# Optimization experiments

Measured on AMD Instinct MI355X. Metric: run time of the kernel, lower is better.

## Reference

```python
import jax, jax.numpy as jnp
import numpy as np

N_NODES = 50000
N_EDGES = 800000
IN_DIM = 9
HIDDEN = 256
N_CAND = 4096


def setup_inputs() -> dict:
    key = jax.random.key(0)
    ks = jax.random.split(key, 12)
    x = jax.random.normal(ks[0], (N_NODES, IN_DIM), dtype=jnp.float32)
    edge_index = jax.random.randint(ks[1], (2, N_EDGES), 0, N_NODES, dtype=jnp.int64)
    candidate_indices = jax.random.randint(ks[2], (N_CAND,), 0, N_NODES, dtype=jnp.int64)
    # GCNConv weights (glorot-ish scale) and biases
    W1 = jax.random.normal(ks[3], (IN_DIM, HIDDEN), dtype=jnp.float32) / np.sqrt(IN_DIM)
    b1 = jnp.zeros((HIDDEN,), dtype=jnp.float32)
    W2 = jax.random.normal(ks[4], (HIDDEN, HIDDEN), dtype=jnp.float32) / np.sqrt(HIDDEN)
    b2 = jnp.zeros((HIDDEN,), dtype=jnp.float32)
    # score head: Linear(hidden,hidden) -> Tanh -> Linear(hidden,1)
    Wh1 = jax.random.normal(ks[5], (HIDDEN, HIDDEN), dtype=jnp.float32) / np.sqrt(HIDDEN)
    bh1 = jnp.zeros((HIDDEN,), dtype=jnp.float32)
    Wh2 = jax.random.normal(ks[6], (HIDDEN, 1), dtype=jnp.float32) / np.sqrt(HIDDEN)
    bh2 = jnp.zeros((1,), dtype=jnp.float32)
    return {"x": x, "W1": W1, "b1": b1, "W2": W2, "b2": b2,
            "Wh1": Wh1, "bh1": bh1, "Wh2": Wh2, "bh2": bh2,
            "edge_index": edge_index, "candidate_indices": candidate_indices}


def _gcn_norm(edge_index, n_nodes):
    # PyG GCNConv default: add self-loops, symmetric normalization D^-1/2 (A+I) D^-1/2
    loop = jnp.arange(n_nodes, dtype=edge_index.dtype)
    src = jnp.concatenate([edge_index[0], loop])
    dst = jnp.concatenate([edge_index[1], loop])
    deg = jax.ops.segment_sum(jnp.ones_like(dst, dtype=jnp.float32), dst,
                              num_segments=n_nodes)
    dinv = jnp.where(deg > 0, jax.lax.rsqrt(deg), 0.0)
    norm = dinv[src] * dinv[dst]  # [E+N]
    return src, dst, norm


def _gcn_layer(h, src, dst, norm, W, b, n_nodes):
    m = h @ W                              # [N, H] dense GEMM first (fewer edge features)
    msg = m[src] * norm[:, None]           # gather + scale: [E+N, H]
    agg = jax.ops.segment_sum(msg, dst, num_segments=n_nodes)  # scatter-add
    return jax.nn.relu(agg + b)


def reference(x, W1, b1, W2, b2, Wh1, bh1, Wh2, bh2, edge_index, candidate_indices):
    n = x.shape[0]
    src, dst, norm = _gcn_norm(edge_index, n)
    h = _gcn_layer(x, src, dst, norm, W1, b1, n)
    h = _gcn_layer(h, src, dst, norm, W2, b2, n)
    cand_h = h[candidate_indices]                       # [K, H]
    scores = (jnp.tanh(cand_h @ Wh1 + bh1) @ Wh2 + bh2).squeeze(-1)  # [K]
    return scores
```

## Files before the change

### kernel.cpp

```cpp
#include <hip/hip_runtime.h>
#include <math.h>

#define N_NODES 50000
#define N_EDGES 800000
#define IN_DIM  9
#define HIDDEN  256
#define N_CAND  4096

#define SCAN_TPB 256
#define SCAN_NB  ((N_NODES + SCAN_TPB - 1) / SCAN_TPB)


__global__ void hist_kernel(const int* __restrict__ dst, int* __restrict__ cnt) {
    int base = (blockIdx.x * blockDim.x + threadIdx.x) * 4;
    if (base >= N_EDGES) return;
    int4 d4 = *(const int4*)(dst + base);
    atomicAdd(&cnt[d4.x], 1);
    atomicAdd(&cnt[d4.y], 1);
    atomicAdd(&cnt[d4.z], 1);
    atomicAdd(&cnt[d4.w], 1);
}

__global__ __launch_bounds__(SCAN_TPB) void scan1_kernel(const int* __restrict__ cnt,
                                                         int* __restrict__ row_ptr,
                                                         int* __restrict__ blockSums) {
    __shared__ int s[SCAN_TPB];
    int t = threadIdx.x;
    int i = blockIdx.x * SCAN_TPB + t;
    int v = (i < N_NODES) ? cnt[i] : 0;
    s[t] = v;
    __syncthreads();
#pragma unroll
    for (int off = 1; off < SCAN_TPB; off <<= 1) {
        int u = (t >= off) ? s[t - off] : 0;
        __syncthreads();
        s[t] += u;
        __syncthreads();
    }
    if (i < N_NODES) row_ptr[i] = s[t] - v;
    if (t == SCAN_TPB - 1) blockSums[blockIdx.x] = s[t];
}

__global__ __launch_bounds__(SCAN_TPB) void scan2_kernel(const int* __restrict__ blockSums,
                                                         int* __restrict__ blockOff,
                                                         int* __restrict__ row_ptr) {
    __shared__ int s[SCAN_TPB];
    int t = threadIdx.x;
    int v = (t < SCAN_NB) ? blockSums[t] : 0;
    s[t] = v;
    __syncthreads();
#pragma unroll
    for (int off = 1; off < SCAN_TPB; off <<= 1) {
        int u = (t >= off) ? s[t - off] : 0;
        __syncthreads();
        s[t] += u;
        __syncthreads();
    }
    if (t < SCAN_NB) blockOff[t] = s[t] - v;
    if (t == SCAN_TPB - 1) row_ptr[N_NODES] = s[t];
}

__global__ __launch_bounds__(SCAN_TPB) void scan3_kernel(const int* __restrict__ cnt,
                                                         const int* __restrict__ blockOff,
                                                         int* __restrict__ row_ptr,
                                                         int* __restrict__ cur,
                                                         float* __restrict__ dinv) {
    int i = blockIdx.x * SCAN_TPB + threadIdx.x;
    if (i < N_NODES) {
        int rp = row_ptr[i] + blockOff[blockIdx.x];
        row_ptr[i] = rp;
        cur[i] = rp;
        dinv[i] = 1.0f / sqrtf((float)(cnt[i] + 1));
    }
}

__global__ void fill_kernel(const int* __restrict__ srcv, const int* __restrict__ dstv,
                            int* __restrict__ cur, int* __restrict__ col) {
    int base = (blockIdx.x * blockDim.x + threadIdx.x) * 4;
    if (base >= N_EDGES) return;
    int4 d4 = *(const int4*)(dstv + base);
    int4 s4 = *(const int4*)(srcv + base);
    int p0 = atomicAdd(&cur[d4.x], 1);
    int p1 = atomicAdd(&cur[d4.y], 1);
    int p2 = atomicAdd(&cur[d4.z], 1);
    int p3 = atomicAdd(&cur[d4.w], 1);
    col[p0] = s4.x;
    col[p1] = s4.y;
    col[p2] = s4.z;
    col[p3] = s4.w;
}


__global__ __launch_bounds__(256) void aggx_kernel(const float* __restrict__ x,
                                                   const int* __restrict__ row_ptr,
                                                   const int* __restrict__ col,
                                                   const float* __restrict__ dinv,
                                                   float* __restrict__ ax) {
    int tid  = threadIdx.x;
    int node = blockIdx.x * 16 + (tid >> 4);
    int l    = tid & 15;
    if (node >= N_NODES) return;

    float a[IN_DIM];
#pragma unroll
    for (int d = 0; d < IN_DIM; ++d) a[d] = 0.f;

    int beg = row_ptr[node], end = row_ptr[node + 1];
    for (int j = beg + l; j < end; j += 16) {
        int s = col[j];
        float w = dinv[s];
        const float* xs = x + (size_t)s * IN_DIM;
#pragma unroll
        for (int d = 0; d < IN_DIM; ++d) a[d] += w * xs[d];
    }

#pragma unroll
    for (int m = 8; m >= 1; m >>= 1) {
#pragma unroll
        for (int d = 0; d < IN_DIM; ++d) a[d] += __shfl_xor(a[d], m);
    }

    float di = dinv[node];
    const float* xi = x + (size_t)node * IN_DIM;
    float o[IN_DIM];
#pragma unroll
    for (int d = 0; d < IN_DIM; ++d) o[d] = di * (di * xi[d] + a[d]);

    float v = o[0];
    if (l == 1) v = o[1];
    if (l == 2) v = o[2];
    if (l == 3) v = o[3];
    if (l == 4) v = o[4];
    if (l == 5) v = o[5];
    if (l == 6) v = o[6];
    if (l == 7) v = o[7];
    if (l == 8) v = o[8];
    if (l < IN_DIM) ax[(size_t)node * IN_DIM + l] = v;
}


#define NPB 8
__global__ __launch_bounds__(256) void h1_kernel(const float* __restrict__ ax,
                                                 const float* __restrict__ W1,
                                                 const float* __restrict__ b1,
                                                 float* __restrict__ h1) {
    int n0 = blockIdx.x * NPB;
    int c = threadIdx.x;
    __shared__ float s[NPB][IN_DIM];
    if (c < NPB * IN_DIM) s[c / IN_DIM][c % IN_DIM] = ax[(size_t)n0 * IN_DIM + c];
    __syncthreads();
    float w[IN_DIM];
#pragma unroll
    for (int k = 0; k < IN_DIM; ++k) w[k] = W1[k * HIDDEN + c];
    float b = b1[c];
#pragma unroll
    for (int r = 0; r < NPB; ++r) {
        float acc = b;
#pragma unroll
        for (int k = 0; k < IN_DIM; ++k) acc += s[r][k] * w[k];
        h1[(size_t)(n0 + r) * HIDDEN + c] = fmaxf(acc, 0.f);
    }
}


__global__ __launch_bounds__(256) void aggc_kernel(const float* __restrict__ h1,
                                                   const int* __restrict__ cand,
                                                   const int* __restrict__ row_ptr,
                                                   const int* __restrict__ col,
                                                   const float* __restrict__ dinv,
                                                   float* __restrict__ g) {
    int k = blockIdx.x * 4 + (threadIdx.x >> 6);
    if (k >= N_CAND) return;
    int lane = threadIdx.x & 63;
    int node = cand[k];
    const float di = dinv[node];
    float4 v = ((const float4*)(h1 + (size_t)node * HIDDEN))[lane];
    float4 acc = make_float4(di * v.x, di * v.y, di * v.z, di * v.w);
    int j = row_ptr[node], end = row_ptr[node + 1];
    for (; j < end; ++j) {
        int s = col[j];
        float w = dinv[s];
        float4 mv = ((const float4*)(h1 + (size_t)s * HIDDEN))[lane];
        acc.x += w * mv.x; acc.y += w * mv.y; acc.z += w * mv.z; acc.w += w * mv.w;
    }
    float4 o = make_float4(di * acc.x, di * acc.y, di * acc.z, di * acc.w);
    ((float4*)(g + (size_t)k * HIDDEN))[lane] = o;
}


#define CPB 2
__global__ __launch_bounds__(256) void head_fused_kernel(const float* __restrict__ g,
                                                         const float* __restrict__ W2,
                                                         const float* __restrict__ b2,
                                                         const float* __restrict__ Wh1,
                                                         const float* __restrict__ bh1,
                                                         const float* __restrict__ Wh2,
                                                         const float* __restrict__ bh2,
                                                         float* __restrict__ out) {
    __shared__ float A[CPB][HIDDEN];
    __shared__ float B[CPB][HIDDEN];
    __shared__ float red[CPB][4];
    int k0 = blockIdx.x * CPB;
    int c = threadIdx.x;

#pragma unroll
    for (int r = 0; r < CPB; ++r) A[r][c] = g[(size_t)(k0 + r) * HIDDEN + c];
    __syncthreads();

    float acc[CPB];
    {
        float b = b2[c];
#pragma unroll
        for (int r = 0; r < CPB; ++r) acc[r] = b;
        for (int i = 0; i < HIDDEN; i += 4) {
            float w0 = W2[(i + 0) * HIDDEN + c];
            float w1 = W2[(i + 1) * HIDDEN + c];
            float w2 = W2[(i + 2) * HIDDEN + c];
            float w3 = W2[(i + 3) * HIDDEN + c];
#pragma unroll
            for (int r = 0; r < CPB; ++r) {
                float4 a = *(const float4*)&A[r][i];
                acc[r] += a.x * w0 + a.y * w1 + a.z * w2 + a.w * w3;
            }
        }
#pragma unroll
        for (int r = 0; r < CPB; ++r) B[r][c] = fmaxf(acc[r], 0.f);
    }
    __syncthreads();

    {
        float b = bh1[c];
#pragma unroll
        for (int r = 0; r < CPB; ++r) acc[r] = b;
        for (int i = 0; i < HIDDEN; i += 4) {
            float w0 = Wh1[(i + 0) * HIDDEN + c];
            float w1 = Wh1[(i + 1) * HIDDEN + c];
            float w2 = Wh1[(i + 2) * HIDDEN + c];
            float w3 = Wh1[(i + 3) * HIDDEN + c];
#pragma unroll
            for (int r = 0; r < CPB; ++r) {
                float4 a = *(const float4*)&B[r][i];
                acc[r] += a.x * w0 + a.y * w1 + a.z * w2 + a.w * w3;
            }
        }
        float w2c = Wh2[c];
#pragma unroll
        for (int r = 0; r < CPB; ++r) acc[r] = tanhf(acc[r]) * w2c;
    }

#pragma unroll
    for (int r = 0; r < CPB; ++r) {
        float v = acc[r];
#pragma unroll
        for (int off = 32; off > 0; off >>= 1) v += __shfl_down(v, off);
        if ((c & 63) == 0) red[r][c >> 6] = v;
    }
    __syncthreads();
    if (c < CPB) out[k0 + c] = red[c][0] + red[c][1] + red[c][2] + red[c][3] + bh2[0];
}


extern "C" void kernel_launch(void* const* d_in, const int* in_sizes, int n_in,
                              void* d_out, int out_size, void* d_ws, size_t ws_size,
                              hipStream_t stream) {
    const float* x   = (const float*)d_in[0];
    const float* W1  = (const float*)d_in[1];
    const float* b1  = (const float*)d_in[2];
    const float* W2  = (const float*)d_in[3];
    const float* b2  = (const float*)d_in[4];
    const float* Wh1 = (const float*)d_in[5];
    const float* bh1 = (const float*)d_in[6];
    const float* Wh2 = (const float*)d_in[7];
    const float* bh2 = (const float*)d_in[8];
    const int* edge_index = (const int*)d_in[9];
    const int* cand       = (const int*)d_in[10];
    float* out = (float*)d_out;

    char* ws = (char*)d_ws;
    size_t off = 0;
    auto alloc = [&](size_t bytes) -> void* {
        void* p = ws + off;
        off += (bytes + 255) & ~(size_t)255;
        return p;
    };
    int*   cnt       = (int*)alloc((size_t)N_NODES * 4);
    int*   row_ptr   = (int*)alloc((size_t)(N_NODES + 1) * 4);
    int*   cur       = (int*)alloc((size_t)N_NODES * 4);
    float* dinv      = (float*)alloc((size_t)N_NODES * 4);
    int*   blockSums = (int*)alloc((size_t)SCAN_NB * 4);
    int*   blockOff  = (int*)alloc((size_t)SCAN_NB * 4);
    int*   col       = (int*)alloc((size_t)N_EDGES * 4);
    float* ax        = (float*)alloc((size_t)N_NODES * IN_DIM * 4);
    float* h1        = (float*)alloc((size_t)N_NODES * HIDDEN * 4);
    float* g         = (float*)alloc((size_t)N_CAND * HIDDEN * 4);

    const int* src = edge_index;
    const int* dst = edge_index + N_EDGES;

    hipMemsetAsync(cnt, 0, (size_t)N_NODES * 4, stream);

    const int E4B = (N_EDGES / 4 + 255) / 256;
    hist_kernel<<<E4B, 256, 0, stream>>>(dst, cnt);
    scan1_kernel<<<SCAN_NB, SCAN_TPB, 0, stream>>>(cnt, row_ptr, blockSums);
    scan2_kernel<<<1, SCAN_TPB, 0, stream>>>(blockSums, blockOff, row_ptr);
    scan3_kernel<<<SCAN_NB, SCAN_TPB, 0, stream>>>(cnt, blockOff, row_ptr, cur, dinv);
    fill_kernel<<<E4B, 256, 0, stream>>>(src, dst, cur, col);

    aggx_kernel<<<(N_NODES + 15) / 16, 256, 0, stream>>>(x, row_ptr, col, dinv, ax);
    h1_kernel<<<N_NODES / NPB, 256, 0, stream>>>(ax, W1, b1, h1);
    aggc_kernel<<<(N_CAND + 3) / 4, 256, 0, stream>>>(h1, cand, row_ptr, col, dinv, g);
    head_fused_kernel<<<N_CAND / CPB, 256, 0, stream>>>(g, W2, b2, Wh1, bh1, Wh2, bh2, out);
}
```

Baseline: 264.2 us.

## Register-tile head MLP with 16 candidates per block and 4x4 thread tiles

Rewrites the fused head kernel so each block processes 16 candidates and each thread computes a 4x4 output tile using float4 weight loads. This reuses each weight load across four rows instead of two per block, cutting global/L2 weight traffic roughly eightfold. The intermediate activations reuse the same shared buffer, and the final reduction is done per wave without a cross-wave shared step. The grid shrinks to 256 blocks, which may leave less parallelism to hide latency.

```diff
diff --git a/kernel.cpp b/kernel.cpp
--- a/kernel.cpp
+++ b/kernel.cpp
@@ -188,7 +188,7 @@
 }
 
 
-#define CPB 2
+#define TM 16
 __global__ __launch_bounds__(256) void head_fused_kernel(const float* __restrict__ g,
                                                          const float* __restrict__ W2,
                                                          const float* __restrict__ b2,
@@ -197,66 +197,82 @@
                                                          const float* __restrict__ Wh2,
                                                          const float* __restrict__ bh2,
                                                          float* __restrict__ out) {
-    __shared__ float A[CPB][HIDDEN];
-    __shared__ float B[CPB][HIDDEN];
-    __shared__ float red[CPB][4];
-    int k0 = blockIdx.x * CPB;
-    int c = threadIdx.x;
-
-#pragma unroll
-    for (int r = 0; r < CPB; ++r) A[r][c] = g[(size_t)(k0 + r) * HIDDEN + c];
-    __syncthreads();
-
-    float acc[CPB];
+    __shared__ float A[TM][HIDDEN];
+    int tid = threadIdx.x;
+    int k0 = blockIdx.x * TM;
+    int rw = (tid >> 6) * 4;
+    int c0 = (tid & 63) * 4;
+
     {
-        float b = b2[c];
-#pragma unroll
-        for (int r = 0; r < CPB; ++r) acc[r] = b;
-        for (int i = 0; i < HIDDEN; i += 4) {
-            float w0 = W2[(i + 0) * HIDDEN + c];
-            float w1 = W2[(i + 1) * HIDDEN + c];
-            float w2 = W2[(i + 2) * HIDDEN + c];
-            float w3 = W2[(i + 3) * HIDDEN + c];
-#pragma unroll
-            for (int r = 0; r < CPB; ++r) {
-                float4 a = *(const float4*)&A[r][i];
-                acc[r] += a.x * w0 + a.y * w1 + a.z * w2 + a.w * w3;
-            }
+        const float4* gp = (const float4*)(g + (size_t)k0 * HIDDEN);
+        float4* Ap = (float4*)&A[0][0];
+#pragma unroll
+        for (int it = 0; it < (TM * HIDDEN / 4) / 256; ++it)
+            Ap[tid + it * 256] = gp[tid + it * 256];
+    }
+    __syncthreads();
+
+    float acc[4][4];
+
+    {
+        float4 bb = *(const float4*)(b2 + c0);
+#pragma unroll
+        for (int i = 0; i < 4; ++i) {
+            acc[i][0] = bb.x; acc[i][1] = bb.y; acc[i][2] = bb.z; acc[i][3] = bb.w;
         }
-#pragma unroll
-        for (int r = 0; r < CPB; ++r) B[r][c] = fmaxf(acc[r], 0.f);
+        for (int k = 0; k < HIDDEN; ++k) {
+            float4 w = *(const float4*)(W2 + (size_t)k * HIDDEN + c0);
+            float a0 = A[rw + 0][k], a1 = A[rw + 1][k];
+            float a2 = A[rw + 2][k], a3 = A[rw + 3][k];
+            acc[0][0] += a0 * w.x; acc[0][1] += a0 * w.y; acc[0][2] += a0 * w.z; acc[0][3] += a0 * w.w;
+            acc[1][0] += a1 * w.x; acc[1][1] += a1 * w.y; acc[1][2] += a1 * w.z; acc[1][3] += a1 * w.w;
+            acc[2][0] += a2 * w.x; acc[2][1] += a2 * w.y; acc[2][2] += a2 * w.z; acc[2][3] += a2 * w.w;
+            acc[3][0] += a3 * w.x; acc[3][1] += a3 * w.y; acc[3][2] += a3 * w.z; acc[3][3] += a3 * w.w;
+        }
+    }
+    __syncthreads();
+#pragma unroll
+    for (int i = 0; i < 4; ++i) {
+        float4 v;
+        v.x = fmaxf(acc[i][0], 0.f); v.y = fmaxf(acc[i][1], 0.f);
+        v.z = fmaxf(acc[i][2], 0.f); v.w = fmaxf(acc[i][3], 0.f);
+        *(float4*)&A[rw + i][c0] = v;
     }
     __syncthreads();
 
     {
-        float b = bh1[c];
-#pragma unroll
-        for (int r = 0; r < CPB; ++r) acc[r] = b;
-        for (int i = 0; i < HIDDEN; i += 4) {
-            float w0 = Wh1[(i + 0) * HIDDEN + c];
-            float w1 = Wh1[(i + 1) * HIDDEN + c];
-            float w2 = Wh1[(i + 2) * HIDDEN + c];
-            float w3 = Wh1[(i + 3) * HIDDEN + c];
-#pragma unroll
-            for (int r = 0; r < CPB; ++r) {
-                float4 a = *(const float4*)&B[r][i];
-                acc[r] += a.x * w0 + a.y * w1 + a.z * w2 + a.w * w3;
-            }
+        float4 bb = *(const float4*)(bh1 + c0);
+#pragma unroll
+        for (int i = 0; i < 4; ++i) {
+            acc[i][0] = bb.x; acc[i][1] = bb.y; acc[i][2] = bb.z; acc[i][3] = bb.w;
         }
-        float w2c = Wh2[c];
-#pragma unroll
-        for (int r = 0; r < CPB; ++r) acc[r] = tanhf(acc[r]) * w2c;
-    }
-
-#pragma unroll
-    for (int r = 0; r < CPB; ++r) {
-        float v = acc[r];
-#pragma unroll
-        for (int off = 32; off > 0; off >>= 1) v += __shfl_down(v, off);
-        if ((c & 63) == 0) red[r][c >> 6] = v;
-    }
-    __syncthreads();
-    if (c < CPB) out[k0 + c] = red[c][0] + red[c][1] + red[c][2] + red[c][3] + bh2[0];
+        for (int k = 0; k < HIDDEN; ++k) {
+            float4 w = *(const float4*)(Wh1 + (size_t)k * HIDDEN + c0);
+            float a0 = A[rw + 0][k], a1 = A[rw + 1][k];
+            float a2 = A[rw + 2][k], a3 = A[rw + 3][k];
+            acc[0][0] += a0 * w.x; acc[0][1] += a0 * w.y; acc[0][2] += a0 * w.z; acc[0][3] += a0 * w.w;
+            acc[1][0] += a1 * w.x; acc[1][1] += a1 * w.y; acc[1][2] += a1 * w.z; acc[1][3] += a1 * w.w;
+            acc[2][0] += a2 * w.x; acc[2][1] += a2 * w.y; acc[2][2] += a2 * w.z; acc[2][3] += a2 * w.w;
+            acc[3][0] += a3 * w.x; acc[3][1] += a3 * w.y; acc[3][2] += a3 * w.z; acc[3][3] += a3 * w.w;
+        }
+    }
+    float4 w2v = *(const float4*)(Wh2 + c0);
+    float s[4];
+#pragma unroll
+    for (int i = 0; i < 4; ++i)
+        s[i] = tanhf(acc[i][0]) * w2v.x + tanhf(acc[i][1]) * w2v.y +
+               tanhf(acc[i][2]) * w2v.z + tanhf(acc[i][3]) * w2v.w;
+
+#pragma unroll
+    for (int off = 32; off > 0; off >>= 1) {
+#pragma unroll
+        for (int i = 0; i < 4; ++i) s[i] += __shfl_down(s[i], off);
+    }
+    if ((tid & 63) == 0) {
+        float b = bh2[0];
+#pragma unroll
+        for (int i = 0; i < 4; ++i) out[k0 + rw + i] = s[i] + b;
+    }
 }
 
 
@@ -309,5 +325,5 @@
     aggx_kernel<<<(N_NODES + 15) / 16, 256, 0, stream>>>(x, row_ptr, col, dinv, ax);
     h1_kernel<<<N_NODES / NPB, 256, 0, stream>>>(ax, W1, b1, h1);
     aggc_kernel<<<(N_CAND + 3) / 4, 256, 0, stream>>>(h1, cand, row_ptr, col, dinv, g);
-    head_fused_kernel<<<N_CAND / CPB, 256, 0, stream>>>(g, W2, b2, Wh1, bh1, Wh2, bh2, out);
-}
+    head_fused_kernel<<<N_CAND / TM, 256, 0, stream>>>(g, W2, b2, Wh1, bh1, Wh2, bh2, out);
+}
```

After: 272.8 us. 3.3% more time.
